# Kernel optimization log

Measured on AMD Instinct MI355X. Metric: run time of the kernel, lower is better.

Reference implementation:

```python
import jax, jax.numpy as jnp
import numpy as np

B, T, D = 128, 197, 768          # batch, tokens, model dim
HEADS, HID_PER_HEAD = 12, 64
H = HEADS * HID_PER_HEAD         # lstm hidden size (== D by construction)


def _block_mask(in_per_head, hid_per_head, head_num):
    """Block-diagonal mask replicated over the 4 LSTM gates (i,f,g,o)."""
    Ht = hid_per_head * head_num
    Dt = in_per_head * head_num
    m = np.zeros((4 * Ht, Dt), np.float32)
    for h in range(head_num):
        for g in range(4):
            r0 = g * Ht + h * hid_per_head
            m[r0:r0 + hid_per_head, h * in_per_head:(h + 1) * in_per_head] = 1.0
    return jnp.asarray(m)


def setup_inputs() -> dict:
    key = jax.random.key(0)
    ks = jax.random.split(key, 16)
    s = 1.0 / np.sqrt(H)  # pytorch LSTM init scale
    u = lambda k, shape: jax.random.uniform(k, shape, jnp.float32, -s, s)
    mask_ih = _block_mask(D // HEADS, HID_PER_HEAD, HEADS)   # [4H, D]
    mask_hh = _block_mask(HID_PER_HEAD, HID_PER_HEAD, HEADS)  # [4H, H]
    inp = {
        "x": jax.random.normal(ks[0], (B, T, D), jnp.float32),
        "pre_w": u(ks[1], (D, D)),
        "pre_b": u(ks[2], (D,)),
        "w_ih_f": u(ks[3], (4 * H, D)) * mask_ih,
        "w_hh_f": u(ks[4], (4 * H, H)) * mask_hh,
        "b_ih_f": u(ks[5], (4 * H,)),
        "b_hh_f": u(ks[6], (4 * H,)),
        "w_ih_r": u(ks[7], (4 * H, D)) * mask_ih,
        "w_hh_r": u(ks[8], (4 * H, H)) * mask_hh,
        "b_ih_r": u(ks[9], (4 * H,)),
        "b_hh_r": u(ks[10], (4 * H,)),
        "proj_w": u(ks[11], (D, 2 * H)),
        "proj_b": u(ks[12], (D,)),
    }
    return inp


def _lstm_dir(x, w_ih, w_hh, b_ih, b_hh, reverse):
    # Precompute input contribution for all timesteps: [B,T,4H]
    xg = jnp.einsum('btd,gd->btg', x, w_ih) + b_ih + b_hh
    xs = jnp.swapaxes(xg, 0, 1)  # [T,B,4H]
    Bn = x.shape[0]

    def step(carry, gx):
        h, c = carry
        gates = gx + h @ w_hh.T
        i, f, g, o = jnp.split(gates, 4, axis=-1)  # pytorch gate order i,f,g,o
        i = jax.nn.sigmoid(i)
        f = jax.nn.sigmoid(f)
        g = jnp.tanh(g)
        o = jax.nn.sigmoid(o)
        c = f * c + i * g
        h = o * jnp.tanh(c)
        return (h, c), h

    init = (jnp.zeros((Bn, w_hh.shape[1]), x.dtype),
            jnp.zeros((Bn, w_hh.shape[1]), x.dtype))
    _, hs = jax.lax.scan(step, init, xs, reverse=reverse)  # outputs aligned to input order
    return jnp.swapaxes(hs, 0, 1)  # [B,T,H]


def reference(x, pre_w, pre_b, w_ih_f, w_hh_f, b_ih_f, b_hh_f,
              w_ih_r, w_hh_r, b_ih_r, b_hh_r, proj_w, proj_b):
    x = x @ pre_w.T + pre_b                      # pre_proj
    hf = _lstm_dir(x, w_ih_f, w_hh_f, b_ih_f, b_hh_f, reverse=False)
    hr = _lstm_dir(x, w_ih_r, w_hh_r, b_ih_r, b_hh_r, reverse=True)
    lstm_out = jnp.concatenate([hf, hr], axis=-1)  # [B,T,2H]
    return lstm_out @ proj_w.T + proj_b            # proj -> [B,T,D]
```

## Files before the change

### kernel.cpp

```cpp
#include <hip/hip_runtime.h>
#include <stdint.h>


#define DEV __device__ __forceinline__

typedef __attribute__((ext_vector_type(8))) short short8;
typedef __attribute__((ext_vector_type(4))) float floatx4;

#define BATCH 128
#define TT    197
#define DD    768
#define NH    12
#define NROWS (BATCH*TT)
#define G4H   3072
#define MT8   99
#define NT8   3

DEV uint16_t f2bf(float f) {
    union { float f; uint32_t u; } v; v.f = f;
    uint32_t r = (v.u + 0x7FFF + ((v.u >> 16) & 1)) >> 16;
    return (uint16_t)r;
}

DEV floatx4 mfma16(short8 a, short8 b, floatx4 c) {
    return __builtin_amdgcn_mfma_f32_16x16x32_bf16(a, b, c, 0, 0, 0);
}

DEV float sigf(float x)   { return __builtin_amdgcn_rcpf(1.0f + __expf(-x)); }
DEV float tanhf_(float x) { return 1.0f - 2.0f * __builtin_amdgcn_rcpf(1.0f + __expf(2.0f * x)); }

DEV void async16(const uint16_t* g, uint16_t* l) {
    __builtin_amdgcn_global_load_lds(
        (const __attribute__((address_space(1))) unsigned int*)g,
        (__attribute__((address_space(3))) unsigned int*)l,
        16, 0, 0);
}

#define CFENCE() asm volatile("" ::: "memory")
#define WAITCNT_LGKM0_ONLY 0xC07F
#define WAITCNT_VM4        0x0F74
#define WAITCNT_VM0        0x0F70

struct CvtArgs {
    const float* src[7];
    uint16_t*    dst[7];
    int          n4[7];
    int          nseg;
};

__global__ void cvt_multi(CvtArgs a) {
    int tid = blockIdx.x * blockDim.x + threadIdx.x;
    int stride = gridDim.x * blockDim.x;
    for (int s = 0; s < a.nseg; s++) {
        const float4* src = (const float4*)a.src[s];
        ushort4* dst = (ushort4*)a.dst[s];
        int n4 = a.n4[s];
        for (int i = tid; i < n4; i += stride) {
            float4 v = src[i];
            ushort4 o;
            o.x = f2bf(v.x); o.y = f2bf(v.y); o.z = f2bf(v.z); o.w = f2bf(v.w);
            dst[i] = o;
        }
    }
}

#define PH_BAR() do { CFENCE(); __builtin_amdgcn_s_barrier(); CFENCE(); } while(0)

#define MFMA_QUAD(QM, QN) do { \
    __builtin_amdgcn_s_setprio(1); \
    _Pragma("unroll") \
    for (int ii = 0; ii < 4; ii++) \
        _Pragma("unroll") \
        for (int j = 0; j < 2; j++) { \
            acc[(QM)*4+ii][(QN)*2+j] = mfma16(af[ii][0], bfr[QN][j][0], acc[(QM)*4+ii][(QN)*2+j]); \
            acc[(QM)*4+ii][(QN)*2+j] = mfma16(af[ii][1], bfr[QN][j][1], acc[(QM)*4+ii][(QN)*2+j]); \
        } \
    __builtin_amdgcn_s_setprio(0); \
} while(0)

template<int STORE_BF16, int LAYOUT>
__global__ __launch_bounds__(512, 2) void gemm256q(
    const uint16_t* __restrict__ A,
    const uint16_t* __restrict__ Bw,
    const float*    __restrict__ bias,
    void*           __restrict__ C,
    int K, int Ntot)
{
    __shared__ __attribute__((aligned(16))) uint16_t lds[65536];

    const int nwg = gridDim.x;
    const int qq = nwg >> 3, rr = nwg & 7;
    const int xcd = blockIdx.x & 7, loc = blockIdx.x >> 3;
    const int swz = (xcd < rr ? xcd*(qq+1) : rr*(qq+1) + (xcd-rr)*qq) + loc;
    const int mt_ = swz / NT8, nt_ = swz - mt_*NT8;
    const int m0 = mt_*256, n0 = nt_*256;

    const int tid  = threadIdx.x;
    const int wv   = tid >> 6;
    const int lane = tid & 63;
    const int ln   = lane & 15;
    const int q    = lane >> 4;
    const int wm   = wv >> 2;
    const int wnx  = wv & 3;
    const int NKT  = K >> 6;

    floatx4 acc[8][4];
#pragma unroll
    for (int i = 0; i < 8; i++)
#pragma unroll
        for (int j = 0; j < 4; j++) acc[i][j] = (floatx4){0.f, 0.f, 0.f, 0.f};

    const int c0   = wv * 2;
    const int rsub = lane >> 3;
    const int kq8  = 8 * ((lane & 7) ^ rsub);
    uint32_t gA[2][2], gB[2][2];
#pragma unroll
    for (int h = 0; h < 2; h++)
#pragma unroll
        for (int l = 0; l < 2; l++) {
            int row = m0 + h*128 + (c0 + l)*8 + rsub;
            if (row >= NROWS) row = NROWS - 1;
            gA[h][l] = (uint32_t)row * (uint32_t)K + kq8;
            gB[h][l] = (uint32_t)(n0 + h*128 + (c0 + l)*8 + rsub) * (uint32_t)K + kq8;
        }

    const int swzE  = (ln & 7) * 8;
    const int colR0 = (q*8)      ^ swzE;
    const int colR1 = (q*8 + 32) ^ swzE;
    const int aL = (wm*128 + ln)*64;
    const int bL = 32768 + (wnx*64 + ln)*64;

    auto stA = [&](int kt, int h) {
        uint32_t k0 = (kt < NKT) ? (uint32_t)(kt << 6) : 0u;
        uint16_t* d = &lds[(kt & 1)*16384 + h*8192 + c0*512];
        async16(A + gA[h][0] + k0, d);
        async16(A + gA[h][1] + k0, d + 512);
    };
    auto stB = [&](int kt, int h) {
        uint32_t k0 = (kt < NKT) ? (uint32_t)(kt << 6) : 0u;
        uint16_t* d = &lds[32768 + (kt & 1)*16384 + h*8192 + c0*512];
        async16(Bw + gB[h][0] + k0, d);
        async16(Bw + gB[h][1] + k0, d + 512);
    };

    stB(0,0); stB(0,1); stA(0,0); stA(0,1); stB(1,0); stB(1,1);
    CFENCE();
    __builtin_amdgcn_s_waitcnt(WAITCNT_VM4);
    __builtin_amdgcn_s_barrier();
    CFENCE();

    short8 af[4][2];
    short8 bfr[2][2][2];

    for (int tt = 0; tt < NKT; tt++) {
        const int lb = (tt & 1) * 16384;
#pragma unroll
        for (int ii = 0; ii < 4; ii++) {
            af[ii][0] = *(const short8*)&lds[lb + aL + ii*1024 + colR0];
            af[ii][1] = *(const short8*)&lds[lb + aL + ii*1024 + colR1];
        }
#pragma unroll
        for (int j = 0; j < 2; j++) {
            bfr[0][j][0] = *(const short8*)&lds[lb + bL + j*1024 + colR0];
            bfr[0][j][1] = *(const short8*)&lds[lb + bL + j*1024 + colR1];
        }
        stA(tt + 1, 0);
        PH_BAR();
        MFMA_QUAD(0, 0);
        PH_BAR();
#pragma unroll
        for (int j = 0; j < 2; j++) {
            bfr[1][j][0] = *(const short8*)&lds[lb + bL + (2+j)*1024 + colR0];
            bfr[1][j][1] = *(const short8*)&lds[lb + bL + (2+j)*1024 + colR1];
        }
        stA(tt + 1, 1);
        PH_BAR();
        MFMA_QUAD(0, 1);
        PH_BAR();
#pragma unroll
        for (int ii = 0; ii < 4; ii++) {
            af[ii][0] = *(const short8*)&lds[lb + aL + (4+ii)*1024 + colR0];
            af[ii][1] = *(const short8*)&lds[lb + aL + (4+ii)*1024 + colR1];
        }
        stB(tt + 2, 0);
        PH_BAR();
        MFMA_QUAD(1, 0);
        PH_BAR();
        stB(tt + 2, 1);
        CFENCE();
        __builtin_amdgcn_s_waitcnt(WAITCNT_VM4);
        __builtin_amdgcn_s_barrier();
        CFENCE();
        MFMA_QUAD(1, 1);
        PH_BAR();
    }
    __builtin_amdgcn_s_waitcnt(WAITCNT_VM0);

#pragma unroll
    for (int i = 0; i < 8; i++)
#pragma unroll
        for (int jj = 0; jj < 4; jj++) {
            int n = n0 + wnx*64 + jj*16 + ln;
            float bv = bias[n];
#pragma unroll
            for (int r = 0; r < 4; r++) {
                int m = m0 + wm*128 + i*16 + q*4 + r;
                if (m < NROWS) {
                    float val = acc[i][jj][r] + bv;
                    if (LAYOUT == 1) {
                        int b = m / 197; int t = m - b*197;
                        int head = n >> 6; int d = n & 63;
                        size_t off = ((size_t)(t*NH + head)*BATCH + b)*64 + d;
                        ((uint16_t*)C)[off] = f2bf(val);
                    } else {
                        size_t off = (size_t)m * Ntot + n;
                        if (STORE_BF16) ((uint16_t*)C)[off] = f2bf(val);
                        else            ((float*)C)[off]    = val;
                    }
                }
            }
        }
}

__global__ __launch_bounds__(256) void lstm_fused(
    const uint16_t* __restrict__ pre,
    const uint16_t* __restrict__ wih_f, const uint16_t* __restrict__ whh_f,
    const uint16_t* __restrict__ wih_r, const uint16_t* __restrict__ whh_r,
    const float* __restrict__ bih_f, const float* __restrict__ bhh_f,
    const float* __restrict__ bih_r, const float* __restrict__ bhh_r,
    uint16_t* __restrict__ hout)
{
    __shared__ __attribute__((aligned(16))) uint16_t hbuf[2][16][72];

    const int tid  = threadIdx.x;
    const int wv   = tid >> 6;
    const int lane = tid & 63;
    const int ln   = lane & 15;
    const int q    = lane >> 4;
    const int b0   = blockIdx.x * 16;
    const int head = blockIdx.y;
    const int dir  = blockIdx.z;
    const int ub   = wv * 16;

    const uint16_t* wih = dir ? wih_r : wih_f;
    const uint16_t* whh = dir ? whh_r : whh_f;
    const float*    bih = dir ? bih_r : bih_f;
    const float*    bhh = dir ? bhh_r : bhh_f;

    short8 aih[4][2], ahh[4][2];
#pragma unroll
    for (int t = 0; t < 4; t++) {
        size_t row = (size_t)(t*768 + head*64 + ub + ln);
#pragma unroll
        for (int s = 0; s < 2; s++) {
            aih[t][s] = *(const short8*)(wih + row*768 + head*64 + s*32 + q*8);
            ahh[t][s] = *(const short8*)(whh + row*768 + head*64 + s*32 + q*8);
        }
    }
    float biasv[4][4];
#pragma unroll
    for (int t = 0; t < 4; t++)
#pragma unroll
        for (int r = 0; r < 4; r++) {
            int row = t*768 + head*64 + ub + q*4 + r;
            biasv[t][r] = bih[row] + bhh[row];
        }

    for (int i = tid; i < 2*16*72; i += 256) ((uint16_t*)hbuf)[i] = 0;
    float c[4] = {0.f, 0.f, 0.f, 0.f};
    __syncthreads();

    const uint16_t* xbase = pre + (size_t)head*BATCH*64 + (size_t)(b0 + ln)*64 + q*8;
    uint16_t* hw = hout + ((size_t)(b0 + ln)*TT)*1536 + dir*768 + head*64 + ub + q*4;

    int t_cur = dir ? (TT - 1) : 0;
    const int tstep = dir ? -1 : 1;
    size_t xo = (size_t)t_cur * NH * BATCH * 64;
    short8 xv0 = *(const short8*)(xbase + xo);
    short8 xv1 = *(const short8*)(xbase + xo + 32);

    for (int step = 0; step < TT; step++) {
        short8 cx0 = xv0, cx1 = xv1;
        int t_next = t_cur + tstep;
        if (step + 1 < TT) {
            size_t xo2 = (size_t)t_next * NH * BATCH * 64;
            xv0 = *(const short8*)(xbase + xo2);
            xv1 = *(const short8*)(xbase + xo2 + 32);
        }
        const int pb = (step + 1) & 1;
        const int cb = step & 1;
        short8 hb0 = *(const short8*)&hbuf[pb][ln][0*32 + q*8];
        short8 hb1 = *(const short8*)&hbuf[pb][ln][1*32 + q*8];

        floatx4 acc[4];
#pragma unroll
        for (int t = 0; t < 4; t++)
            acc[t] = (floatx4){biasv[t][0], biasv[t][1], biasv[t][2], biasv[t][3]};
#pragma unroll
        for (int t = 0; t < 4; t++) {
            acc[t] = mfma16(aih[t][0], cx0, acc[t]);
            acc[t] = mfma16(ahh[t][0], hb0, acc[t]);
            acc[t] = mfma16(aih[t][1], cx1, acc[t]);
            acc[t] = mfma16(ahh[t][1], hb1, acc[t]);
        }

        float hv[4];
#pragma unroll
        for (int r = 0; r < 4; r++) {
            float ig = sigf(acc[0][r]);
            float fg = sigf(acc[1][r]);
            float gg = tanhf_(acc[2][r]);
            float og = sigf(acc[3][r]);
            c[r] = fg * c[r] + ig * gg;
            hv[r] = og * tanhf_(c[r]);
        }
        uint2 hp;
        asm volatile("v_cvt_pk_bf16_f32 %0, %1, %2" : "=v"(hp.x) : "v"(hv[0]), "v"(hv[1]));
        asm volatile("v_cvt_pk_bf16_f32 %0, %1, %2" : "=v"(hp.y) : "v"(hv[2]), "v"(hv[3]));

        *(uint2*)&hbuf[cb][ln][ub + q*4] = hp;
        *(uint2*)(hw + (size_t)t_cur * 1536) = hp;

        CFENCE();
        __builtin_amdgcn_s_waitcnt(WAITCNT_LGKM0_ONLY);
        __builtin_amdgcn_s_barrier();
        CFENCE();

        t_cur = t_next;
    }
}

extern "C" void kernel_launch(void* const* d_in, const int* in_sizes, int n_in,
                              void* d_out, int out_size, void* d_ws, size_t ws_size,
                              hipStream_t stream) {
    (void)in_sizes; (void)n_in; (void)out_size; (void)ws_size;
    const float* x     = (const float*)d_in[0];
    const float* pre_w = (const float*)d_in[1];
    const float* pre_b = (const float*)d_in[2];
    const float* wihf  = (const float*)d_in[3];
    const float* whhf  = (const float*)d_in[4];
    const float* bihf  = (const float*)d_in[5];
    const float* bhhf  = (const float*)d_in[6];
    const float* wihr  = (const float*)d_in[7];
    const float* whhr  = (const float*)d_in[8];
    const float* bihr  = (const float*)d_in[9];
    const float* bhhr  = (const float*)d_in[10];
    const float* projw = (const float*)d_in[11];
    const float* projb = (const float*)d_in[12];
    float* out = (float*)d_out;

    uint16_t* W = (uint16_t*)d_ws;
    uint16_t* xb     = W; W += (size_t)NROWS * DD;
    uint16_t* bwpre  = W; W += (size_t)DD * DD;
    uint16_t* bwihf  = W; W += (size_t)G4H * DD;
    uint16_t* bwhhf  = W; W += (size_t)G4H * DD;
    uint16_t* bwihr  = W; W += (size_t)G4H * DD;
    uint16_t* bwhhr  = W; W += (size_t)G4H * DD;
    uint16_t* bwproj = W; W += (size_t)DD * 2 * DD;
    uint16_t* preb   = W; W += (size_t)NROWS * DD;
    uint16_t* houtb  = W; W += (size_t)NROWS * 2 * DD;

    CvtArgs ca;
    ca.src[0] = x;     ca.dst[0] = xb;     ca.n4[0] = (int)((size_t)NROWS * DD / 4);
    ca.src[1] = pre_w; ca.dst[1] = bwpre;  ca.n4[1] = DD * DD / 4;
    ca.src[2] = wihf;  ca.dst[2] = bwihf;  ca.n4[2] = G4H * DD / 4;
    ca.src[3] = whhf;  ca.dst[3] = bwhhf;  ca.n4[3] = G4H * DD / 4;
    ca.src[4] = wihr;  ca.dst[4] = bwihr;  ca.n4[4] = G4H * DD / 4;
    ca.src[5] = whhr;  ca.dst[5] = bwhhr;  ca.n4[5] = G4H * DD / 4;
    ca.src[6] = projw; ca.dst[6] = bwproj; ca.n4[6] = DD * 2 * DD / 4;
    ca.nseg = 7;
    hipLaunchKernelGGL(cvt_multi, dim3(1024), dim3(256), 0, stream, ca);

    const int GBLK8 = MT8 * NT8;

    hipLaunchKernelGGL((gemm256q<1, 1>), dim3(GBLK8), dim3(512), 0, stream,
                       xb, bwpre, pre_b, (void*)preb, DD, DD);
    hipLaunchKernelGGL(lstm_fused, dim3(8, 12, 2), dim3(256), 0, stream,
                       preb, bwihf, bwhhf, bwihr, bwhhr,
                       bihf, bhhf, bihr, bhhr, houtb);
    hipLaunchKernelGGL((gemm256q<0, 0>), dim3(GBLK8), dim3(512), 0, stream,
                       houtb, bwproj, projb, (void*)out, 2 * DD, DD);
}
```

Baseline: 477.8 us.

## Precompute next-step input gates off the recurrence path and fold log2e into weights

The LSTM recurrence now computes the input-projection MFMAs for the next timestep after the recurrent MFMAs of the current step. Only the two hidden-state MFMAs per gate remain on the serial dependency chain, and input loads are prefetched three steps ahead. The gate weights and biases are pre-scaled by log2(e), or 2·log2(e) for the tanh gate, during the bf16 conversion, so activations use raw v_exp_f32 without a multiply. The loop is unrolled by two with fixed double-buffer indices. Scaling before bf16 rounding slightly changes numerics.

```diff
diff --git a/kernel.cpp b/kernel.cpp
--- a/kernel.cpp
+++ b/kernel.cpp
@@ -16,6 +16,9 @@
 #define MT8   99
 #define NT8   3
 
+#define LOG2E  1.4426950408889634f
+#define LOG2E2 2.8853900817779268f
+
 DEV uint16_t f2bf(float f) {
     union { float f; uint32_t u; } v; v.f = f;
     uint32_t r = (v.u + 0x7FFF + ((v.u >> 16) & 1)) >> 16;
@@ -26,8 +29,8 @@
     return __builtin_amdgcn_mfma_f32_16x16x32_bf16(a, b, c, 0, 0, 0);
 }
 
-DEV float sigf(float x)   { return __builtin_amdgcn_rcpf(1.0f + __expf(-x)); }
-DEV float tanhf_(float x) { return 1.0f - 2.0f * __builtin_amdgcn_rcpf(1.0f + __expf(2.0f * x)); }
+DEV float exp2pos(float x) { float r; asm("v_exp_f32 %0, %1"  : "=v"(r) : "v"(x)); return r; }
+DEV float exp2neg(float x) { float r; asm("v_exp_f32 %0, -%1" : "=v"(r) : "v"(x)); return r; }
 
 DEV void async16(const uint16_t* g, uint16_t* l) {
     __builtin_amdgcn_global_load_lds(
@@ -45,6 +48,7 @@
     const float* src[7];
     uint16_t*    dst[7];
     int          n4[7];
+    int          gscale[7];
     int          nseg;
 };
 
@@ -55,8 +59,14 @@
         const float4* src = (const float4*)a.src[s];
         ushort4* dst = (ushort4*)a.dst[s];
         int n4 = a.n4[s];
+        int gs = a.gscale[s];
         for (int i = tid; i < n4; i += stride) {
             float4 v = src[i];
+            if (gs) {
+                int gate = i / 147456;
+                float sc = (gate == 2) ? LOG2E2 : LOG2E;
+                v.x *= sc; v.y *= sc; v.z *= sc; v.w *= sc;
+            }
             ushort4 o;
             o.x = f2bf(v.x); o.y = f2bf(v.y); o.z = f2bf(v.z); o.w = f2bf(v.w);
             dst[i] = o;
@@ -222,7 +232,7 @@
         }
 }
 
-__global__ __launch_bounds__(256) void lstm_fused(
+__global__ __launch_bounds__(256, 1) void lstm_fused(
     const uint16_t* __restrict__ pre,
     const uint16_t* __restrict__ wih_f, const uint16_t* __restrict__ whh_f,
     const uint16_t* __restrict__ wih_r, const uint16_t* __restrict__ whh_r,
@@ -257,76 +267,125 @@
             ahh[t][s] = *(const short8*)(whh + row*768 + head*64 + s*32 + q*8);
         }
     }
-    float biasv[4][4];
-#pragma unroll
-    for (int t = 0; t < 4; t++)
+    floatx4 bias4[4];
+#pragma unroll
+    for (int t = 0; t < 4; t++) {
+        const float gsc = (t == 2) ? LOG2E2 : LOG2E;
 #pragma unroll
         for (int r = 0; r < 4; r++) {
             int row = t*768 + head*64 + ub + q*4 + r;
-            biasv[t][r] = bih[row] + bhh[row];
-        }
+            bias4[t][r] = (bih[row] + bhh[row]) * gsc;
+        }
+    }
 
     for (int i = tid; i < 2*16*72; i += 256) ((uint16_t*)hbuf)[i] = 0;
     float c[4] = {0.f, 0.f, 0.f, 0.f};
     __syncthreads();
 
+    const ptrdiff_t XS = (ptrdiff_t)NH * BATCH * 64;
+    const int ts = dir ? -1 : 1;
+    const int t0 = dir ? (TT - 1) : 0;
     const uint16_t* xbase = pre + (size_t)head*BATCH*64 + (size_t)(b0 + ln)*64 + q*8;
-    uint16_t* hw = hout + ((size_t)(b0 + ln)*TT)*1536 + dir*768 + head*64 + ub + q*4;
-
-    int t_cur = dir ? (TT - 1) : 0;
-    const int tstep = dir ? -1 : 1;
-    size_t xo = (size_t)t_cur * NH * BATCH * 64;
-    short8 xv0 = *(const short8*)(xbase + xo);
-    short8 xv1 = *(const short8*)(xbase + xo + 32);
-
-    for (int step = 0; step < TT; step++) {
-        short8 cx0 = xv0, cx1 = xv1;
-        int t_next = t_cur + tstep;
-        if (step + 1 < TT) {
-            size_t xo2 = (size_t)t_next * NH * BATCH * 64;
-            xv0 = *(const short8*)(xbase + xo2);
-            xv1 = *(const short8*)(xbase + xo2 + 32);
-        }
-        const int pb = (step + 1) & 1;
-        const int cb = step & 1;
-        short8 hb0 = *(const short8*)&hbuf[pb][ln][0*32 + q*8];
-        short8 hb1 = *(const short8*)&hbuf[pb][ln][1*32 + q*8];
-
-        floatx4 acc[4];
-#pragma unroll
-        for (int t = 0; t < 4; t++)
-            acc[t] = (floatx4){biasv[t][0], biasv[t][1], biasv[t][2], biasv[t][3]};
+    uint16_t* hst = hout + ((size_t)(b0 + ln)*TT)*1536 + dir*768 + head*64 + ub + q*4
+                    + (ptrdiff_t)t0 * 1536;
+    const ptrdiff_t HSTEP = (ptrdiff_t)ts * 1536;
+
+    floatx4 xacc[4];
+    {
+        const uint16_t* xp = xbase + (ptrdiff_t)t0 * XS;
+        short8 x0 = *(const short8*)xp;
+        short8 x1 = *(const short8*)(xp + 32);
 #pragma unroll
         for (int t = 0; t < 4; t++) {
-            acc[t] = mfma16(aih[t][0], cx0, acc[t]);
-            acc[t] = mfma16(ahh[t][0], hb0, acc[t]);
-            acc[t] = mfma16(aih[t][1], cx1, acc[t]);
-            acc[t] = mfma16(ahh[t][1], hb1, acc[t]);
-        }
+            xacc[t] = bias4[t];
+            xacc[t] = mfma16(aih[t][0], x0, xacc[t]);
+            xacc[t] = mfma16(aih[t][1], x1, xacc[t]);
+        }
+    }
+    short8 xa0, xa1, xb0, xb1;
+    {
+        const uint16_t* p1 = xbase + (ptrdiff_t)(t0 + ts) * XS;
+        const uint16_t* p2 = xbase + (ptrdiff_t)(t0 + 2*ts) * XS;
+        xa0 = *(const short8*)p1; xa1 = *(const short8*)(p1 + 32);
+        xb0 = *(const short8*)p2; xb1 = *(const short8*)(p2 + 32);
+    }
+    const uint16_t* xload = xbase + (ptrdiff_t)(t0 + 3*ts) * XS;
+    const ptrdiff_t XSTEP = (ptrdiff_t)ts * XS;
+
+    auto body = [&](int s, short8& nx0, short8& nx1, int PB, int CB) {
+        short8 hb0 = *(const short8*)&hbuf[PB][ln][q*8];
+        short8 hb1 = *(const short8*)&hbuf[PB][ln][32 + q*8];
+        floatx4 g[4];
+#pragma unroll
+        for (int t = 0; t < 4; t++) {
+            g[t] = mfma16(ahh[t][0], hb0, xacc[t]);
+            g[t] = mfma16(ahh[t][1], hb1, g[t]);
+        }
+#pragma unroll
+        for (int t = 0; t < 4; t++) {
+            xacc[t] = bias4[t];
+            xacc[t] = mfma16(aih[t][0], nx0, xacc[t]);
+            xacc[t] = mfma16(aih[t][1], nx1, xacc[t]);
+        }
+        if (s + 3 < TT) {
+            nx0 = *(const short8*)xload;
+            nx1 = *(const short8*)(xload + 32);
+        }
+        xload += XSTEP;
 
         float hv[4];
 #pragma unroll
         for (int r = 0; r < 4; r++) {
-            float ig = sigf(acc[0][r]);
-            float fg = sigf(acc[1][r]);
-            float gg = tanhf_(acc[2][r]);
-            float og = sigf(acc[3][r]);
-            c[r] = fg * c[r] + ig * gg;
-            hv[r] = og * tanhf_(c[r]);
+            float ig = __builtin_amdgcn_rcpf(1.f + exp2neg(g[0][r]));
+            float fg = __builtin_amdgcn_rcpf(1.f + exp2neg(g[1][r]));
+            float gg = 1.f - 2.f*__builtin_amdgcn_rcpf(1.f + exp2pos(g[2][r]));
+            float og = __builtin_amdgcn_rcpf(1.f + exp2neg(g[3][r]));
+            c[r] = fg*c[r] + ig*gg;
+            float th = 1.f - 2.f*__builtin_amdgcn_rcpf(1.f + exp2pos(c[r]*LOG2E2));
+            hv[r] = og*th;
         }
         uint2 hp;
         asm volatile("v_cvt_pk_bf16_f32 %0, %1, %2" : "=v"(hp.x) : "v"(hv[0]), "v"(hv[1]));
         asm volatile("v_cvt_pk_bf16_f32 %0, %1, %2" : "=v"(hp.y) : "v"(hv[2]), "v"(hv[3]));
 
-        *(uint2*)&hbuf[cb][ln][ub + q*4] = hp;
-        *(uint2*)(hw + (size_t)t_cur * 1536) = hp;
+        *(uint2*)&hbuf[CB][ln][ub + q*4] = hp;
+        *(uint2*)hst = hp;
+        hst += HSTEP;
 
         CFENCE();
         __builtin_amdgcn_s_waitcnt(WAITCNT_LGKM0_ONLY);
         __builtin_amdgcn_s_barrier();
         CFENCE();
-
-        t_cur = t_next;
+    };
+
+    for (int s = 0; s < TT - 1; s += 2) {
+        body(s,     xa0, xa1, 1, 0);
+        body(s + 1, xb0, xb1, 0, 1);
+    }
+    {
+        short8 hb0 = *(const short8*)&hbuf[1][ln][q*8];
+        short8 hb1 = *(const short8*)&hbuf[1][ln][32 + q*8];
+        floatx4 g[4];
+#pragma unroll
+        for (int t = 0; t < 4; t++) {
+            g[t] = mfma16(ahh[t][0], hb0, xacc[t]);
+            g[t] = mfma16(ahh[t][1], hb1, g[t]);
+        }
+        float hv[4];
+#pragma unroll
+        for (int r = 0; r < 4; r++) {
+            float ig = __builtin_amdgcn_rcpf(1.f + exp2neg(g[0][r]));
+            float fg = __builtin_amdgcn_rcpf(1.f + exp2neg(g[1][r]));
+            float gg = 1.f - 2.f*__builtin_amdgcn_rcpf(1.f + exp2pos(g[2][r]));
+            float og = __builtin_amdgcn_rcpf(1.f + exp2neg(g[3][r]));
+            c[r] = fg*c[r] + ig*gg;
+            float th = 1.f - 2.f*__builtin_amdgcn_rcpf(1.f + exp2pos(c[r]*LOG2E2));
+            hv[r] = og*th;
+        }
+        uint2 hp;
+        asm volatile("v_cvt_pk_bf16_f32 %0, %1, %2" : "=v"(hp.x) : "v"(hv[0]), "v"(hv[1]));
+        asm volatile("v_cvt_pk_bf16_f32 %0, %1, %2" : "=v"(hp.y) : "v"(hv[2]), "v"(hv[3]));
+        *(uint2*)hst = hp;
     }
 }
 
@@ -361,13 +420,13 @@
     uint16_t* houtb  = W; W += (size_t)NROWS * 2 * DD;
 
     CvtArgs ca;
-    ca.src[0] = x;     ca.dst[0] = xb;     ca.n4[0] = (int)((size_t)NROWS * DD / 4);
-    ca.src[1] = pre_w; ca.dst[1] = bwpre;  ca.n4[1] = DD * DD / 4;
-    ca.src[2] = wihf;  ca.dst[2] = bwihf;  ca.n4[2] = G4H * DD / 4;
-    ca.src[3] = whhf;  ca.dst[3] = bwhhf;  ca.n4[3] = G4H * DD / 4;
-    ca.src[4] = wihr;  ca.dst[4] = bwihr;  ca.n4[4] = G4H * DD / 4;
-    ca.src[5] = whhr;  ca.dst[5] = bwhhr;  ca.n4[5] = G4H * DD / 4;
-    ca.src[6] = projw; ca.dst[6] = bwproj; ca.n4[6] = DD * 2 * DD / 4;
+    ca.src[0] = x;     ca.dst[0] = xb;     ca.n4[0] = (int)((size_t)NROWS * DD / 4); ca.gscale[0] = 0;
+    ca.src[1] = pre_w; ca.dst[1] = bwpre;  ca.n4[1] = DD * DD / 4;                    ca.gscale[1] = 0;
+    ca.src[2] = wihf;  ca.dst[2] = bwihf;  ca.n4[2] = G4H * DD / 4;                   ca.gscale[2] = 1;
+    ca.src[3] = whhf;  ca.dst[3] = bwhhf;  ca.n4[3] = G4H * DD / 4;                   ca.gscale[3] = 1;
+    ca.src[4] = wihr;  ca.dst[4] = bwihr;  ca.n4[4] = G4H * DD / 4;                   ca.gscale[4] = 1;
+    ca.src[5] = whhr;  ca.dst[5] = bwhhr;  ca.n4[5] = G4H * DD / 4;                   ca.gscale[5] = 1;
+    ca.src[6] = projw; ca.dst[6] = bwproj; ca.n4[6] = DD * 2 * DD / 4;                ca.gscale[6] = 0;
     ca.nseg = 7;
     hipLaunchKernelGGL(cvt_multi, dim3(1024), dim3(256), 0, stream, ca);
 
```

Result: faster. 462.2 us (-3.3%).
